# Optimization experiments

Hardware: AMD Instinct MI355X
Metric: run time of the kernel (lower is better)

Reference implementation:

```python
import jax, jax.numpy as jnp
import numpy as np

# init_kwargs constants
ALPHA = 0.1
BETA = 0.1
CAPACITY = 1000.0
IDX_LNN = 0   # feat_idx['ln(N+1)']
IDX_DOBS = 2  # feat_idx['D_observed']
IDX_RATE = 3  # feat_idx['pkt_rate']

N = 4_194_304
W = 4096  # number of windows (static upper bound on window ids)
EPS = 1e-6


def _masked_quantile75(vals, valid):
    """torch.quantile(vals[valid], 0.75) with linear interpolation, jit-safe."""
    s = jnp.sort(jnp.where(valid, vals, jnp.inf))
    n = jnp.sum(valid)
    pos = jnp.maximum(0.75 * (n - 1).astype(jnp.float32), 0.0)
    lo = jnp.floor(pos).astype(jnp.int32)
    hi = jnp.ceil(pos).astype(jnp.int32)
    frac = pos - lo.astype(jnp.float32)
    q = s[lo] * (1.0 - frac) + s[hi] * frac
    return jnp.where(n > 0, jnp.maximum(q, EPS), 1.0)


def setup_inputs() -> dict:
    key = jax.random.key(0)
    k1, k2, k3, k4, k5 = jax.random.split(key, 5)
    logits = jax.random.normal(k1, (N, 2), jnp.float32)
    y = jax.random.randint(k2, (N,), 0, 2)
    mask = jnp.ones((N,), bool)
    x_raw = jax.random.normal(k3, (N, 4), jnp.float32)
    window_idx = jax.random.randint(k4, (N,), 0, W)
    class_weights = jax.random.uniform(k5, (2,), jnp.float32, 0.5, 1.5)
    return {"logits": logits, "y": y, "mask": mask, "x_raw": x_raw,
            "window_idx": window_idx, "class_weights": class_weights}


def reference(logits, y, mask, x_raw, window_idx, class_weights):
    maskf = mask.astype(jnp.float32)
    any_mask = jnp.sum(maskf) > 0

    # L_data: weighted cross entropy over masked samples
    logp = jax.nn.log_softmax(logits, axis=1)
    nll = -jnp.take_along_axis(logp, y[:, None], axis=1)[:, 0]
    wy = class_weights[y]
    denom = jnp.sum(maskf * wy)
    l_data = jnp.sum(maskf * wy * nll) / jnp.maximum(denom, 1e-12)

    # per-window physics terms (vectorized segment reductions)
    valid = (window_idx >= 0) & mask
    vf = valid.astype(jnp.float32)
    attack_prob = jax.nn.softmax(logits, axis=1)[:, 1]
    flow_rate = jnp.maximum(x_raw[:, IDX_RATE], 0.0)
    d_obs = jnp.maximum(x_raw[:, IDX_DOBS], 0.0)
    # note: flow_vol (exp(lnN)-1) is computed in the original but never used in the loss

    ref_dobs = _masked_quantile75(d_obs, valid)

    seg = jnp.where(valid, window_idx, 0).astype(jnp.int32)
    pv = attack_prob * vf  # zeroed contributions for invalid rows
    cnt = jax.ops.segment_sum(vf, seg, num_segments=W)
    sum_p = jax.ops.segment_sum(pv, seg, num_segments=W)
    agg_rate = jax.ops.segment_sum(pv * flow_rate, seg, num_segments=W)
    sum_pd = jax.ops.segment_sum(pv * d_obs, seg, num_segments=W)

    include = ((cnt >= 2.0) & (sum_p >= EPS)).astype(jnp.float32)

    d_mean = sum_pd / (sum_p + EPS)
    rate_ratio = agg_rate / (CAPACITY + EPS)
    buildup = jax.nn.relu(rate_ratio - 1.0)
    flow_t = buildup * buildup
    rho = jnp.clip(rate_ratio, 0.0, 0.99)
    d_theory = 1.0 / (1.0 - rho + EPS)
    lat_t = jax.nn.relu(d_theory - d_mean / ref_dobs)

    n_inc = jnp.sum(include)
    safe_n = jnp.maximum(n_inc, 1.0)
    l_flow = jnp.where(n_inc > 0, jnp.sum(flow_t * include) / safe_n, 0.0)
    l_latency = jnp.where(n_inc > 0, jnp.sum(lat_t * include) / safe_n, 0.0)

    # empty-mask early return path
    l_data = jnp.where(any_mask, l_data, 0.0)
    l_flow = jnp.where(any_mask, l_flow, 0.0)
    l_latency = jnp.where(any_mask, l_latency, 0.0)
    l_total = l_data + ALPHA * l_flow + BETA * l_latency
    return (l_total, l_data, l_flow, l_latency)
```

## Files before the change

### kernel.cpp

```cpp
#include <hip/hip_runtime.h>

#define NWIN 4096
#define EPSF 1e-6f
#define GRID_MAIN 512
#define BLOCK_MAIN 512
#define NWAVES (BLOCK_MAIN / 64)

#define SCALE_P   2097152.0f
#define SCALE_R   131072.0f
#define INV_P     (1.0/2097152.0)
#define INV_R     (1.0/131072.0)

#define OFF_SEG   256
#define OFF_H1    65792
#define OFF_H2    73984
#define OFF_H3    90368
#define OFF_CEP   98560
#define OFF_SEGU  131072
#define OFF_PART  262144

__device__ __forceinline__ unsigned make_key_raw(const float2* __restrict__ xzw,
                                                 const int* __restrict__ mask,
                                                 const int* __restrict__ widx, int i)
{
    int wi = widx[i];
    int m = mask[i];
    if (wi < 0 || !m) return 0x7F800000u;
    float d = fmaxf(xzw[2 * i + 1].x, 0.0f);
    unsigned k = __float_as_uint(d);
    return (k == 0x80000000u) ? 0u : k;
}

__device__ __forceinline__ void process_elem(
    float lgx, float lgy, int yi, int mi, float xz, float xw, int wi,
    float cw0, float cw1, unsigned* keyOut,
    float& num, float& den, unsigned& nv, unsigned& nm, unsigned& zc,
    unsigned* s_seg, unsigned* s_h1)
{
    float d = lgx - lgy;
    float ad = fabsf(d);
    float t = __expf(-ad);
    float inv1t = 1.0f / (1.0f + t);
    float l1p = __logf(1.0f + t);
    float s = yi ? d : -d;
    float nll = fmaxf(s, 0.0f) + l1p;
    float maskf = mi ? 1.0f : 0.0f;
    float wy = (yi ? cw1 : cw0) * maskf;
    nm += (mi != 0);
    num += wy * nll;
    den += wy;

    bool vq = (wi >= 0) && mi;
    float dob = fmaxf(xz, 0.0f);
    unsigned kraw = __float_as_uint(dob);
    kraw = (kraw == 0x80000000u) ? 0u : kraw;
    unsigned key = vq ? kraw : 0x7F800000u;
    *keyOut = key;
    nv += vq;
    zc += (key == 0u);

    atomicAdd(&s_h1[key >> 21], (key != 0u) ? 1u : 0u);

    bool sv = vq && ((unsigned)wi < NWIN);
    float sf = sv ? 1.0f : 0.0f;
    unsigned b = sv ? ((unsigned)wi << 2) : (4u * NWIN);
    float p = ((d > 0.0f) ? t : 1.0f) * inv1t;
    float rate = fmaxf(xw, 0.0f);
    atomicAdd(&s_seg[b],     sv ? 1u : 0u);
    atomicAdd(&s_seg[b | 1], (unsigned)(sf * p * SCALE_P + 0.5f));
    atomicAdd(&s_seg[b | 2], (unsigned)(sf * p * rate * SCALE_R + 0.5f));
    atomicAdd(&s_seg[b | 3], (unsigned)(sf * p * dob * SCALE_R + 0.5f));
}

extern "C" __global__ __launch_bounds__(BLOCK_MAIN)
void k_main(const float2* __restrict__ logits, const int* __restrict__ y,
            const int* __restrict__ mask, const float2* __restrict__ xzw,
            const int* __restrict__ widx, const float* __restrict__ cw,
            float* __restrict__ ce_part,
            unsigned* __restrict__ g_seg_u32, unsigned* __restrict__ part,
            unsigned* __restrict__ keys, unsigned* __restrict__ gh1,
            int use_part, int use_keys, int n)
{
    __shared__ unsigned s_seg[4 * NWIN + 4];
    __shared__ unsigned s_h1[2048];
    __shared__ float s_redf[2 * NWAVES];
    __shared__ unsigned s_redu[3 * NWAVES];
    for (int j = threadIdx.x; j < 4 * NWIN + 4; j += BLOCK_MAIN) s_seg[j] = 0u;
    for (int j = threadIdx.x; j < 2048; j += BLOCK_MAIN) s_h1[j] = 0u;
    __syncthreads();

    const float cw0 = cw[0], cw1 = cw[1];
    float num = 0.0f, den = 0.0f;
    unsigned nv = 0u, nm = 0u, zc = 0u;

    const int nth = GRID_MAIN * BLOCK_MAIN;
    const int gtid = blockIdx.x * BLOCK_MAIN + threadIdx.x;
    const int nq = n >> 2;

    const float4* lg4 = (const float4*)logits;
    const int4* y4p = (const int4*)y;
    const int4* m4p = (const int4*)mask;
    const int4* w4p = (const int4*)widx;

    for (int q = gtid; q < nq; q += nth) {
        float4 lgA = lg4[2 * q], lgB = lg4[2 * q + 1];
        int4 y4 = y4p[q], m4 = m4p[q], w4 = w4p[q];
        float2 z0 = xzw[8 * q + 1], z1 = xzw[8 * q + 3];
        float2 z2 = xzw[8 * q + 5], z3 = xzw[8 * q + 7];

        uint4 kq;
        process_elem(lgA.x, lgA.y, y4.x, m4.x, z0.x, z0.y, w4.x,
                     cw0, cw1, &kq.x, num, den, nv, nm, zc, s_seg, s_h1);
        process_elem(lgA.z, lgA.w, y4.y, m4.y, z1.x, z1.y, w4.y,
                     cw0, cw1, &kq.y, num, den, nv, nm, zc, s_seg, s_h1);
        process_elem(lgB.x, lgB.y, y4.z, m4.z, z2.x, z2.y, w4.z,
                     cw0, cw1, &kq.z, num, den, nv, nm, zc, s_seg, s_h1);
        process_elem(lgB.z, lgB.w, y4.w, m4.w, z3.x, z3.y, w4.w,
                     cw0, cw1, &kq.w, num, den, nv, nm, zc, s_seg, s_h1);
        if (use_keys) ((uint4*)keys)[q] = kq;
    }
    for (int i = (nq << 2) + gtid; i < n; i += nth) {
        float2 lg = logits[i];
        float2 zz = xzw[2 * i + 1];
        unsigned k;
        process_elem(lg.x, lg.y, y[i], mask[i], zz.x, zz.y, widx[i],
                     cw0, cw1, &k, num, den, nv, nm, zc, s_seg, s_h1);
        if (use_keys) keys[i] = k;
    }

    for (int off = 32; off > 0; off >>= 1) {
        num += __shfl_down(num, off);
        den += __shfl_down(den, off);
        nv  += __shfl_down(nv, off);
        nm  += __shfl_down(nm, off);
        zc  += __shfl_down(zc, off);
    }
    const int wid = threadIdx.x >> 6;
    if ((threadIdx.x & 63) == 0) {
        s_redf[wid] = num; s_redf[NWAVES + wid] = den;
        s_redu[wid] = nv; s_redu[NWAVES + wid] = nm; s_redu[2 * NWAVES + wid] = zc;
    }
    __syncthreads();
    if (threadIdx.x == 0) {
        float tn = 0.0f, td = 0.0f;
        unsigned ta = 0u, tb = 0u, tc = 0u;
        for (int w = 0; w < NWAVES; ++w) {
            tn += s_redf[w]; td += s_redf[NWAVES + w];
            ta += s_redu[w]; tb += s_redu[NWAVES + w]; tc += s_redu[2 * NWAVES + w];
        }
        float* cp = ce_part + blockIdx.x * 8;
        cp[0] = tn; cp[1] = td;
        ((unsigned*)cp)[2] = ta; ((unsigned*)cp)[3] = tb; ((unsigned*)cp)[4] = tc;
    }

    if (use_part) {
        uint4* dst = (uint4*)(part + (size_t)blockIdx.x * (4 * NWIN));
        const uint4* src = (const uint4*)s_seg;
        for (int j = threadIdx.x; j < NWIN; j += BLOCK_MAIN) dst[j] = src[j];
    } else {
        for (int j = threadIdx.x; j < 4 * NWIN; j += BLOCK_MAIN) {
            unsigned v = s_seg[j];
            if (v) atomicAdd(&g_seg_u32[j], v);
        }
    }
    for (int j = threadIdx.x; j < 2048; j += BLOCK_MAIN) {
        unsigned v = s_h1[j];
        if (v) atomicAdd(&gh1[j], v);
    }
}

extern "C" __global__ __launch_bounds__(512)
void k_cefin(const float* __restrict__ ce_part, double* __restrict__ ws_d,
             unsigned* __restrict__ ws_u, unsigned* __restrict__ gh1)
{
    __shared__ double sd[2 * 8];
    __shared__ unsigned su[3 * 8];
    const int tid = threadIdx.x;
    const float* cp = ce_part + tid * 8;
    double n_ = (double)cp[0];
    double d_ = (double)cp[1];
    unsigned a = ((const unsigned*)cp)[2];
    unsigned b = ((const unsigned*)cp)[3];
    unsigned c = ((const unsigned*)cp)[4];
    for (int off = 32; off > 0; off >>= 1) {
        n_ += __shfl_down(n_, off);
        d_ += __shfl_down(d_, off);
        a  += __shfl_down(a, off);
        b  += __shfl_down(b, off);
        c  += __shfl_down(c, off);
    }
    const int wid = tid >> 6;
    if ((tid & 63) == 0) { sd[wid] = n_; sd[8 + wid] = d_;
                           su[wid] = a; su[8 + wid] = b; su[16 + wid] = c; }
    __syncthreads();
    if (tid == 0) {
        double tn = 0.0, td = 0.0;
        unsigned ta = 0u, tb = 0u, tc = 0u;
        for (int w = 0; w < 8; ++w) {
            tn += sd[w]; td += sd[8 + w];
            ta += su[w]; tb += su[8 + w]; tc += su[16 + w];
        }
        ws_d[0] = tn; ws_d[1] = td;
        ws_u[4] = ta; ws_u[5] = tb;
        gh1[0] += tc;
    }
}

extern "C" __global__ __launch_bounds__(256)
void k_reduce(const unsigned* __restrict__ part, unsigned* __restrict__ g_seg_u32)
{
    const int bin = (blockIdx.x & 63) * 256 + threadIdx.x;
    const int c = blockIdx.x >> 6;
    const unsigned* p = part + (size_t)c * (GRID_MAIN / 4) * (4 * NWIN) + bin;
    unsigned s = 0u;
#pragma unroll 8
    for (int b = 0; b < GRID_MAIN / 4; ++b) s += p[(size_t)b * (4 * NWIN)];
    if (s) atomicAdd(&g_seg_u32[bin], s);
}

extern "C" __global__ __launch_bounds__(256)
void k_convert(const unsigned* __restrict__ gsu, float* __restrict__ g_seg)
{
    const int j = blockIdx.x * 256 + threadIdx.x;
    const int c = j & 3;
    double inv = (c == 0) ? 1.0 : (c == 1) ? INV_P : INV_R;
    g_seg[j] = (float)((double)gsu[j] * inv);
}

__device__ __forceinline__ void h2_one(unsigned key, unsigned p0, unsigned p1,
                                       unsigned* h)
{
    unsigned top = key >> 21;
    unsigned sub = (key >> 10) & 2047u;
    if (top == p0) atomicAdd(&h[sub], 1u);
    if (top == p1) atomicAdd(&h[2048 + sub], 1u);
}

extern "C" __global__ __launch_bounds__(256)
void k_hist2(const unsigned* __restrict__ keys, const float2* __restrict__ xzw,
             const int* __restrict__ mask, const int* __restrict__ widx,
             int use_keys, int n, const unsigned* __restrict__ ws_u,
             unsigned* __restrict__ gh)
{
    __shared__ unsigned h[2 * 2048];
    for (int j = threadIdx.x; j < 2 * 2048; j += 256) h[j] = 0u;
    __syncthreads();
    const unsigned p0 = ws_u[8], p1 = ws_u[9];
    const int nthr = gridDim.x * blockDim.x;
    const int gtid = blockIdx.x * blockDim.x + threadIdx.x;
    const int nq = n >> 2;
    if (use_keys) {
        const uint4* k4 = (const uint4*)keys;
        int base = gtid;
        for (; base + 3 * nthr < nq; base += 4 * nthr) {
            uint4 a = k4[base], b = k4[base + nthr];
            uint4 c = k4[base + 2 * nthr], d = k4[base + 3 * nthr];
            h2_one(a.x, p0, p1, h); h2_one(a.y, p0, p1, h);
            h2_one(a.z, p0, p1, h); h2_one(a.w, p0, p1, h);
            h2_one(b.x, p0, p1, h); h2_one(b.y, p0, p1, h);
            h2_one(b.z, p0, p1, h); h2_one(b.w, p0, p1, h);
            h2_one(c.x, p0, p1, h); h2_one(c.y, p0, p1, h);
            h2_one(c.z, p0, p1, h); h2_one(c.w, p0, p1, h);
            h2_one(d.x, p0, p1, h); h2_one(d.y, p0, p1, h);
            h2_one(d.z, p0, p1, h); h2_one(d.w, p0, p1, h);
        }
        for (; base < nq; base += nthr) {
            uint4 a = k4[base];
            h2_one(a.x, p0, p1, h); h2_one(a.y, p0, p1, h);
            h2_one(a.z, p0, p1, h); h2_one(a.w, p0, p1, h);
        }
        for (int i = (nq << 2) + gtid; i < n; i += nthr)
            h2_one(keys[i], p0, p1, h);
    } else {
        for (int i = gtid; i < n; i += nthr)
            h2_one(make_key_raw(xzw, mask, widx, i), p0, p1, h);
    }
    __syncthreads();
    for (int j = threadIdx.x; j < 2 * 2048; j += 256)
        if (h[j]) atomicAdd(&gh[j], h[j]);
}

__device__ __forceinline__ void h3_one(unsigned key, unsigned p0, unsigned p1,
                                       unsigned* h)
{
    unsigned top = key >> 10;
    unsigned sub = key & 1023u;
    if (top == p0) atomicAdd(&h[sub], 1u);
    if (top == p1) atomicAdd(&h[1024 + sub], 1u);
}

extern "C" __global__ __launch_bounds__(256)
void k_hist3(const unsigned* __restrict__ keys, const float2* __restrict__ xzw,
             const int* __restrict__ mask, const int* __restrict__ widx,
             int use_keys, int n, const unsigned* __restrict__ ws_u,
             unsigned* __restrict__ gh)
{
    __shared__ unsigned h[2 * 1024];
    for (int j = threadIdx.x; j < 2 * 1024; j += 256) h[j] = 0u;
    __syncthreads();
    const unsigned p0 = ws_u[8], p1 = ws_u[9];
    const int nthr = gridDim.x * blockDim.x;
    const int gtid = blockIdx.x * blockDim.x + threadIdx.x;
    const int nq = n >> 2;
    if (use_keys) {
        const uint4* k4 = (const uint4*)keys;
        int base = gtid;
        for (; base + 3 * nthr < nq; base += 4 * nthr) {
            uint4 a = k4[base], b = k4[base + nthr];
            uint4 c = k4[base + 2 * nthr], d = k4[base + 3 * nthr];
            h3_one(a.x, p0, p1, h); h3_one(a.y, p0, p1, h);
            h3_one(a.z, p0, p1, h); h3_one(a.w, p0, p1, h);
            h3_one(b.x, p0, p1, h); h3_one(b.y, p0, p1, h);
            h3_one(b.z, p0, p1, h); h3_one(b.w, p0, p1, h);
            h3_one(c.x, p0, p1, h); h3_one(c.y, p0, p1, h);
            h3_one(c.z, p0, p1, h); h3_one(c.w, p0, p1, h);
            h3_one(d.x, p0, p1, h); h3_one(d.y, p0, p1, h);
            h3_one(d.z, p0, p1, h); h3_one(d.w, p0, p1, h);
        }
        for (; base < nq; base += nthr) {
            uint4 a = k4[base];
            h3_one(a.x, p0, p1, h); h3_one(a.y, p0, p1, h);
            h3_one(a.z, p0, p1, h); h3_one(a.w, p0, p1, h);
        }
        for (int i = (nq << 2) + gtid; i < n; i += nthr)
            h3_one(keys[i], p0, p1, h);
    } else {
        for (int i = gtid; i < n; i += nthr)
            h3_one(make_key_raw(xzw, mask, widx, i), p0, p1, h);
    }
    __syncthreads();
    for (int j = threadIdx.x; j < 2 * 1024; j += 256)
        if (h[j]) atomicAdd(&gh[j], h[j]);
}

__device__ void scan_search(const unsigned* __restrict__ gh, int NB, unsigned rank,
                            unsigned* sv, unsigned* wsb, unsigned* ret)
{
    const int tid = threadIdx.x;
    for (int j = tid; j < NB; j += 256) sv[j] = gh[j];
    __syncthreads();
    const int E = NB >> 8;
    const int base = tid * E;
    unsigned loc = 0u;
    for (int e = 0; e < E; ++e) loc += sv[base + e];
    unsigned inc = loc;
    const int lane = tid & 63;
    for (int off = 1; off < 64; off <<= 1) {
        unsigned u = __shfl_up(inc, off);
        if (lane >= off) inc += u;
    }
    const int wid = tid >> 6;
    if (lane == 63) wsb[wid] = inc;
    __syncthreads();
    if (tid == 0) {
        unsigned run = 0u;
        for (int w = 0; w < 4; ++w) { unsigned t = wsb[w]; wsb[w] = run; run += t; }
    }
    __syncthreads();
    unsigned c = wsb[wid] + (inc - loc);
    for (int e = 0; e < E; ++e) {
        unsigned hv = sv[base + e];
        if (rank >= c && rank < c + hv) { ret[0] = (unsigned)(base + e); ret[1] = rank - c; }
        c += hv;
    }
    __syncthreads();
}

extern "C" __global__ __launch_bounds__(256)
void k_scan1(unsigned* __restrict__ ws_u, float* __restrict__ ws_f,
             const unsigned* __restrict__ gh)
{
    __shared__ unsigned sv[2048];
    __shared__ unsigned wsb[4];
    __shared__ unsigned ret[2];
    __shared__ unsigned rk[2];
    if (threadIdx.x == 0) {
        int n = (int)ws_u[4];
        float nf = (float)(n - 1);
        float pos = fmaxf(0.75f * nf, 0.0f);
        float lo = floorf(pos);
        ws_f[7] = pos - lo;
        rk[0] = (unsigned)lo;
        rk[1] = (unsigned)ceilf(pos);
    }
    __syncthreads();
    unsigned r0 = rk[0], r1 = rk[1];
    scan_search(gh, 2048, r0, sv, wsb, ret);
    if (threadIdx.x == 0) { ws_u[8] = ret[0]; ws_u[10] = ret[1]; }
    scan_search(gh, 2048, r1, sv, wsb, ret);
    if (threadIdx.x == 0) { ws_u[9] = ret[0]; ws_u[11] = ret[1]; }
}

extern "C" __global__ __launch_bounds__(256)
void k_scan2(unsigned* __restrict__ ws_u, const unsigned* __restrict__ gh)
{
    __shared__ unsigned sv[2048];
    __shared__ unsigned wsb[4];
    __shared__ unsigned ret[2];
    unsigned p0 = ws_u[8], p1 = ws_u[9];
    unsigned r0 = ws_u[10], r1 = ws_u[11];
    scan_search(gh, 2048, r0, sv, wsb, ret);
    if (threadIdx.x == 0) { ws_u[8] = (p0 << 11) | ret[0]; ws_u[10] = ret[1]; }
    scan_search(gh + 2048, 2048, r1, sv, wsb, ret);
    if (threadIdx.x == 0) { ws_u[9] = (p1 << 11) | ret[0]; ws_u[11] = ret[1]; }
}

extern "C" __global__ __launch_bounds__(256)
void k_scan3(unsigned* __restrict__ ws_u, float* __restrict__ ws_f,
             const unsigned* __restrict__ gh)
{
    __shared__ unsigned sv[2048];
    __shared__ unsigned wsb[4];
    __shared__ unsigned ret[2];
    unsigned p0 = ws_u[8], p1 = ws_u[9];
    unsigned r0 = ws_u[10], r1 = ws_u[11];
    scan_search(gh, 1024, r0, sv, wsb, ret);
    float v0 = __uint_as_float((p0 << 10) | ret[0]);
    scan_search(gh + 1024, 1024, r1, sv, wsb, ret);
    float v1 = __uint_as_float((p1 << 10) | ret[0]);
    if (threadIdx.x == 0) {
        int n = (int)ws_u[4];
        float frac = ws_f[7];
        float q = v0 * (1.0f - frac) + v1 * frac;
        ws_f[6] = (n > 0) ? fmaxf(q, EPSF) : 1.0f;
    }
}

extern "C" __global__ __launch_bounds__(1024)
void k_final(const float* __restrict__ g_seg, const double* __restrict__ ws_d,
             const float* __restrict__ ws_f, const unsigned* __restrict__ ws_u,
             float* __restrict__ out)
{
    __shared__ double red[48];
    const double ref = (double)ws_f[6];
    const float4* gs4 = (const float4*)g_seg;
    double ninc = 0.0, fsum = 0.0, lsum = 0.0;
    for (int w = threadIdx.x; w < NWIN; w += blockDim.x) {
        float4 v = gs4[w];
        double c   = (double)v.x;
        double sp  = (double)v.y;
        double ar  = (double)v.z;
        double spd = (double)v.w;
        double inc = (c >= 2.0 && sp >= 1e-6) ? 1.0 : 0.0;
        double dmean = spd / (sp + 1e-6);
        double rr = ar / (1000.0 + 1e-6);
        double bu = fmax(rr - 1.0, 0.0);
        double flow = bu * bu;
        double rho = fmin(fmax(rr, 0.0), 0.99);
        double dth = 1.0 / (1.0 - rho + 1e-6);
        double lat = fmax(dth - dmean / ref, 0.0);
        ninc += inc; fsum += flow * inc; lsum += lat * inc;
    }
    for (int off = 32; off > 0; off >>= 1) {
        ninc += __shfl_down(ninc, off);
        fsum += __shfl_down(fsum, off);
        lsum += __shfl_down(lsum, off);
    }
    int wid = threadIdx.x >> 6, lane = threadIdx.x & 63;
    if (lane == 0) { red[wid] = ninc; red[16 + wid] = fsum; red[32 + wid] = lsum; }
    __syncthreads();
    if (threadIdx.x == 0) {
        double n_i = 0.0, f_s = 0.0, l_s = 0.0;
        int nw = (int)blockDim.x >> 6;
        for (int w = 0; w < nw; ++w) { n_i += red[w]; f_s += red[16 + w]; l_s += red[32 + w]; }
        double safe = fmax(n_i, 1.0);
        double l_flow = (n_i > 0.0) ? f_s / safe : 0.0;
        double l_lat  = (n_i > 0.0) ? l_s / safe : 0.0;
        double den = ws_d[1];
        double l_data = ws_d[0] / fmax(den, 1e-12);
        bool any = ws_u[5] > 0u;
        if (!any) { l_data = 0.0; l_flow = 0.0; l_lat = 0.0; }
        out[0] = (float)(l_data + 0.1 * l_flow + 0.1 * l_lat);
        out[1] = (float)l_data;
        out[2] = (float)l_flow;
        out[3] = (float)l_lat;
    }
}

extern "C" void kernel_launch(void* const* d_in, const int* in_sizes, int n_in,
                              void* d_out, int out_size, void* d_ws, size_t ws_size,
                              hipStream_t stream)
{
    const float2* logits = (const float2*)d_in[0];
    const int* y = (const int*)d_in[1];
    const int* mask = (const int*)d_in[2];
    const float2* xzw = (const float2*)d_in[3];
    const int* widx = (const int*)d_in[4];
    const float* cw = (const float*)d_in[5];
    float* out = (float*)d_out;
    const int n = in_sizes[1];

    unsigned char* ws8 = (unsigned char*)d_ws;
    double* ws_d = (double*)ws8;
    float* ws_f = (float*)ws8;
    unsigned* ws_u = (unsigned*)ws8;
    float* g_seg = (float*)(ws8 + OFF_SEG);
    unsigned* g_h1 = (unsigned*)(ws8 + OFF_H1);
    unsigned* g_h2 = (unsigned*)(ws8 + OFF_H2);
    unsigned* g_h3 = (unsigned*)(ws8 + OFF_H3);
    float* ce_part = (float*)(ws8 + OFF_CEP);
    unsigned* g_seg_u32 = (unsigned*)(ws8 + OFF_SEGU);

    const size_t part_bytes = (size_t)GRID_MAIN * 4 * NWIN * 4;
    const size_t keys_bytes = (size_t)n * 4u;
    size_t off = OFF_PART;
    int use_part = 0, use_keys = 0;
    unsigned* part = (unsigned*)(ws8 + off);
    if (ws_size >= off + part_bytes) { use_part = 1; off += part_bytes; }
    unsigned* keys = (unsigned*)(ws8 + off);
    if (ws_size >= off + keys_bytes) { use_keys = 1; }

    hipMemsetAsync(d_ws, 0, OFF_PART, stream);

    k_main<<<GRID_MAIN, BLOCK_MAIN, 0, stream>>>(logits, y, mask, xzw, widx, cw,
                                                 ce_part, g_seg_u32, part, keys,
                                                 g_h1, use_part, use_keys, n);
    k_cefin<<<1, 512, 0, stream>>>(ce_part, ws_d, ws_u, g_h1);
    if (use_part)
        k_reduce<<<256, 256, 0, stream>>>(part, g_seg_u32);
    k_convert<<<64, 256, 0, stream>>>(g_seg_u32, g_seg);
    k_scan1<<<1, 256, 0, stream>>>(ws_u, ws_f, g_h1);
    k_hist2<<<1024, 256, 0, stream>>>(keys, xzw, mask, widx, use_keys, n, ws_u, g_h2);
    k_scan2<<<1, 256, 0, stream>>>(ws_u, g_h2);
    k_hist3<<<1024, 256, 0, stream>>>(keys, xzw, mask, widx, use_keys, n, ws_u, g_h3);
    k_scan3<<<1, 256, 0, stream>>>(ws_u, ws_f, g_h3);
    k_final<<<1, 1024, 0, stream>>>(g_seg, ws_d, ws_f, ws_u, out);
}
```

Baseline: 98.80 us.

## Fuse post-processing kernels to cut launch count in the quantile pipeline

Merges k_cefin, k_reduce, k_convert and k_scan1 into a single k_post launch, where 128 blocks reduce the per-block partial window sums and one extra block does the cross-entropy finalisation and the first histogram scan. k_scan3 and k_convert are folded into k_final, which now scans the third histogram itself and converts the fixed-point window sums inline. This removes four kernel launches and their serial gaps. The cost is that k_post's reduction now uses 128 blocks of 512 threads instead of 256 blocks of 256, and the zero-count correction to the first histogram is applied in shared memory instead of written back to global memory.

Measured after the change: 91.84 us (median of 2 runs). 7.0% less time.

```diff
diff --git a/kernel.cpp b/kernel.cpp
--- a/kernel.cpp
+++ b/kernel.cpp
@@ -11,13 +11,12 @@
 #define INV_P     (1.0/2097152.0)
 #define INV_R     (1.0/131072.0)
 
-#define OFF_SEG   256
+#define OFF_SEGU  256
 #define OFF_H1    65792
 #define OFF_H2    73984
 #define OFF_H3    90368
 #define OFF_CEP   98560
-#define OFF_SEGU  131072
-#define OFF_PART  262144
+#define OFF_PART  131072
 
 __device__ __forceinline__ unsigned make_key_raw(const float2* __restrict__ xzw,
                                                  const int* __restrict__ mask,
@@ -169,12 +168,68 @@
     }
 }
 
+__device__ void scan_search_g(const unsigned* __restrict__ gh, int NB, unsigned rank,
+                              unsigned zadd, unsigned* sv, unsigned* wsb,
+                              unsigned* ret)
+{
+    const int tid = threadIdx.x;
+    const int B = blockDim.x;
+    for (int j = tid; j < NB; j += B) sv[j] = gh[j] + ((j == 0) ? zadd : 0u);
+    __syncthreads();
+    const int E = NB / B;
+    const int base = tid * E;
+    unsigned loc = 0u;
+    for (int e = 0; e < E; ++e) loc += sv[base + e];
+    unsigned inc = loc;
+    const int lane = tid & 63;
+    for (int off = 1; off < 64; off <<= 1) {
+        unsigned u = __shfl_up(inc, off);
+        if (lane >= off) inc += u;
+    }
+    const int wid = tid >> 6;
+    const int nw = B >> 6;
+    if (lane == 63) wsb[wid] = inc;
+    __syncthreads();
+    if (tid == 0) {
+        unsigned run = 0u;
+        for (int w = 0; w < nw; ++w) { unsigned t = wsb[w]; wsb[w] = run; run += t; }
+    }
+    __syncthreads();
+    unsigned c = wsb[wid] + (inc - loc);
+    for (int e = 0; e < E; ++e) {
+        unsigned hv = sv[base + e];
+        if (rank >= c && rank < c + hv) { ret[0] = (unsigned)(base + e); ret[1] = rank - c; }
+        c += hv;
+    }
+    __syncthreads();
+}
+
 extern "C" __global__ __launch_bounds__(512)
-void k_cefin(const float* __restrict__ ce_part, double* __restrict__ ws_d,
-             unsigned* __restrict__ ws_u, unsigned* __restrict__ gh1)
-{
+void k_post(const unsigned* __restrict__ part, unsigned* __restrict__ g_seg_u32,
+            const float* __restrict__ ce_part, double* __restrict__ ws_d,
+            unsigned* __restrict__ ws_u, float* __restrict__ ws_f,
+            const unsigned* __restrict__ gh1, int use_part)
+{
+    if (blockIdx.x < 128) {
+        if (!use_part) return;
+        const int c = blockIdx.x >> 5;
+        const int bin = (blockIdx.x & 31) * 512 + threadIdx.x;
+        const unsigned* p = part + (size_t)c * 128 * (4 * NWIN) + bin;
+        unsigned s = 0u;
+#pragma unroll 8
+        for (int b = 0; b < 128; ++b) s += p[(size_t)b * (4 * NWIN)];
+        if (s) atomicAdd(&g_seg_u32[bin], s);
+        return;
+    }
+
+    __shared__ unsigned sv[2048];
+    __shared__ unsigned wsb[16];
+    __shared__ unsigned ret[2];
     __shared__ double sd[2 * 8];
     __shared__ unsigned su[3 * 8];
+    __shared__ unsigned bc[4];
+    __shared__ float bf[1];
+
     const int tid = threadIdx.x;
     const float* cp = ce_part + tid * 8;
     double n_ = (double)cp[0];
@@ -202,29 +257,24 @@
         }
         ws_d[0] = tn; ws_d[1] = td;
         ws_u[4] = ta; ws_u[5] = tb;
-        gh1[0] += tc;
-    }
-}
-
-extern "C" __global__ __launch_bounds__(256)
-void k_reduce(const unsigned* __restrict__ part, unsigned* __restrict__ g_seg_u32)
-{
-    const int bin = (blockIdx.x & 63) * 256 + threadIdx.x;
-    const int c = blockIdx.x >> 6;
-    const unsigned* p = part + (size_t)c * (GRID_MAIN / 4) * (4 * NWIN) + bin;
-    unsigned s = 0u;
-#pragma unroll 8
-    for (int b = 0; b < GRID_MAIN / 4; ++b) s += p[(size_t)b * (4 * NWIN)];
-    if (s) atomicAdd(&g_seg_u32[bin], s);
-}
-
-extern "C" __global__ __launch_bounds__(256)
-void k_convert(const unsigned* __restrict__ gsu, float* __restrict__ g_seg)
-{
-    const int j = blockIdx.x * 256 + threadIdx.x;
-    const int c = j & 3;
-    double inv = (c == 0) ? 1.0 : (c == 1) ? INV_P : INV_R;
-    g_seg[j] = (float)((double)gsu[j] * inv);
+        float nf = (float)((int)ta - 1);
+        float pos = fmaxf(0.75f * nf, 0.0f);
+        float lo = floorf(pos);
+        bf[0] = pos - lo;
+        bc[0] = tc;
+        bc[1] = ta;
+        bc[2] = (unsigned)lo;
+        bc[3] = (unsigned)ceilf(pos);
+    }
+    __syncthreads();
+    const unsigned zadd = bc[0];
+    const unsigned r0 = bc[2], r1 = bc[3];
+    if (tid == 0) ws_f[7] = bf[0];
+
+    scan_search_g(gh1, 2048, r0, zadd, sv, wsb, ret);
+    if (tid == 0) { ws_u[8] = ret[0]; ws_u[10] = ret[1]; }
+    scan_search_g(gh1, 2048, r1, zadd, sv, wsb, ret);
+    if (tid == 0) { ws_u[9] = ret[0]; ws_u[11] = ret[1]; }
 }
 
 __device__ __forceinline__ void h2_one(unsigned key, unsigned p0, unsigned p1,
@@ -280,6 +330,20 @@
         if (h[j]) atomicAdd(&gh[j], h[j]);
 }
 
+extern "C" __global__ __launch_bounds__(256)
+void k_scan2(unsigned* __restrict__ ws_u, const unsigned* __restrict__ gh)
+{
+    __shared__ unsigned sv[2048];
+    __shared__ unsigned wsb[16];
+    __shared__ unsigned ret[2];
+    unsigned p0 = ws_u[8], p1 = ws_u[9];
+    unsigned r0 = ws_u[10], r1 = ws_u[11];
+    scan_search_g(gh, 2048, r0, 0u, sv, wsb, ret);
+    if (threadIdx.x == 0) { ws_u[8] = (p0 << 11) | ret[0]; ws_u[10] = ret[1]; }
+    scan_search_g(gh + 2048, 2048, r1, 0u, sv, wsb, ret);
+    if (threadIdx.x == 0) { ws_u[9] = (p1 << 11) | ret[0]; ws_u[11] = ret[1]; }
+}
+
 __device__ __forceinline__ void h3_one(unsigned key, unsigned p0, unsigned p1,
                                        unsigned* h)
 {
@@ -333,114 +397,36 @@
         if (h[j]) atomicAdd(&gh[j], h[j]);
 }
 
-__device__ void scan_search(const unsigned* __restrict__ gh, int NB, unsigned rank,
-                            unsigned* sv, unsigned* wsb, unsigned* ret)
-{
-    const int tid = threadIdx.x;
-    for (int j = tid; j < NB; j += 256) sv[j] = gh[j];
-    __syncthreads();
-    const int E = NB >> 8;
-    const int base = tid * E;
-    unsigned loc = 0u;
-    for (int e = 0; e < E; ++e) loc += sv[base + e];
-    unsigned inc = loc;
-    const int lane = tid & 63;
-    for (int off = 1; off < 64; off <<= 1) {
-        unsigned u = __shfl_up(inc, off);
-        if (lane >= off) inc += u;
-    }
-    const int wid = tid >> 6;
-    if (lane == 63) wsb[wid] = inc;
-    __syncthreads();
-    if (tid == 0) {
-        unsigned run = 0u;
-        for (int w = 0; w < 4; ++w) { unsigned t = wsb[w]; wsb[w] = run; run += t; }
-    }
-    __syncthreads();
-    unsigned c = wsb[wid] + (inc - loc);
-    for (int e = 0; e < E; ++e) {
-        unsigned hv = sv[base + e];
-        if (rank >= c && rank < c + hv) { ret[0] = (unsigned)(base + e); ret[1] = rank - c; }
-        c += hv;
-    }
-    __syncthreads();
-}
-
-extern "C" __global__ __launch_bounds__(256)
-void k_scan1(unsigned* __restrict__ ws_u, float* __restrict__ ws_f,
-             const unsigned* __restrict__ gh)
-{
-    __shared__ unsigned sv[2048];
-    __shared__ unsigned wsb[4];
+extern "C" __global__ __launch_bounds__(1024)
+void k_final(const unsigned* __restrict__ g_seg_u32, const double* __restrict__ ws_d,
+             const float* __restrict__ ws_f, const unsigned* __restrict__ ws_u,
+             const unsigned* __restrict__ gh3, float* __restrict__ out)
+{
+    __shared__ unsigned sv[1024];
+    __shared__ unsigned wsb[16];
     __shared__ unsigned ret[2];
-    __shared__ unsigned rk[2];
-    if (threadIdx.x == 0) {
-        int n = (int)ws_u[4];
-        float nf = (float)(n - 1);
-        float pos = fmaxf(0.75f * nf, 0.0f);
-        float lo = floorf(pos);
-        ws_f[7] = pos - lo;
-        rk[0] = (unsigned)lo;
-        rk[1] = (unsigned)ceilf(pos);
-    }
-    __syncthreads();
-    unsigned r0 = rk[0], r1 = rk[1];
-    scan_search(gh, 2048, r0, sv, wsb, ret);
-    if (threadIdx.x == 0) { ws_u[8] = ret[0]; ws_u[10] = ret[1]; }
-    scan_search(gh, 2048, r1, sv, wsb, ret);
-    if (threadIdx.x == 0) { ws_u[9] = ret[0]; ws_u[11] = ret[1]; }
-}
-
-extern "C" __global__ __launch_bounds__(256)
-void k_scan2(unsigned* __restrict__ ws_u, const unsigned* __restrict__ gh)
-{
-    __shared__ unsigned sv[2048];
-    __shared__ unsigned wsb[4];
-    __shared__ unsigned ret[2];
-    unsigned p0 = ws_u[8], p1 = ws_u[9];
-    unsigned r0 = ws_u[10], r1 = ws_u[11];
-    scan_search(gh, 2048, r0, sv, wsb, ret);
-    if (threadIdx.x == 0) { ws_u[8] = (p0 << 11) | ret[0]; ws_u[10] = ret[1]; }
-    scan_search(gh + 2048, 2048, r1, sv, wsb, ret);
-    if (threadIdx.x == 0) { ws_u[9] = (p1 << 11) | ret[0]; ws_u[11] = ret[1]; }
-}
-
-extern "C" __global__ __launch_bounds__(256)
-void k_scan3(unsigned* __restrict__ ws_u, float* __restrict__ ws_f,
-             const unsigned* __restrict__ gh)
-{
-    __shared__ unsigned sv[2048];
-    __shared__ unsigned wsb[4];
-    __shared__ unsigned ret[2];
-    unsigned p0 = ws_u[8], p1 = ws_u[9];
-    unsigned r0 = ws_u[10], r1 = ws_u[11];
-    scan_search(gh, 1024, r0, sv, wsb, ret);
-    float v0 = __uint_as_float((p0 << 10) | ret[0]);
-    scan_search(gh + 1024, 1024, r1, sv, wsb, ret);
-    float v1 = __uint_as_float((p1 << 10) | ret[0]);
-    if (threadIdx.x == 0) {
-        int n = (int)ws_u[4];
-        float frac = ws_f[7];
-        float q = v0 * (1.0f - frac) + v1 * frac;
-        ws_f[6] = (n > 0) ? fmaxf(q, EPSF) : 1.0f;
-    }
-}
-
-extern "C" __global__ __launch_bounds__(1024)
-void k_final(const float* __restrict__ g_seg, const double* __restrict__ ws_d,
-             const float* __restrict__ ws_f, const unsigned* __restrict__ ws_u,
-             float* __restrict__ out)
-{
     __shared__ double red[48];
-    const double ref = (double)ws_f[6];
-    const float4* gs4 = (const float4*)g_seg;
+
+    const unsigned p0 = ws_u[8], p1 = ws_u[9];
+    const unsigned r0 = ws_u[10], r1 = ws_u[11];
+    scan_search_g(gh3, 1024, r0, 0u, sv, wsb, ret);
+    const float v0 = __uint_as_float((p0 << 10) | ret[0]);
+    scan_search_g(gh3 + 1024, 1024, r1, 0u, sv, wsb, ret);
+    const float v1 = __uint_as_float((p1 << 10) | ret[0]);
+
+    const int nvalid = (int)ws_u[4];
+    const float frac = ws_f[7];
+    const float qf = v0 * (1.0f - frac) + v1 * frac;
+    const double ref = (double)((nvalid > 0) ? fmaxf(qf, EPSF) : 1.0f);
+
+    const uint4* gs4 = (const uint4*)g_seg_u32;
     double ninc = 0.0, fsum = 0.0, lsum = 0.0;
     for (int w = threadIdx.x; w < NWIN; w += blockDim.x) {
-        float4 v = gs4[w];
+        uint4 v = gs4[w];
         double c   = (double)v.x;
-        double sp  = (double)v.y;
-        double ar  = (double)v.z;
-        double spd = (double)v.w;
+        double sp  = (double)v.y * INV_P;
+        double ar  = (double)v.z * INV_R;
+        double spd = (double)v.w * INV_R;
         double inc = (c >= 2.0 && sp >= 1e-6) ? 1.0 : 0.0;
         double dmean = spd / (sp + 1e-6);
         double rr = ar / (1000.0 + 1e-6);
@@ -494,12 +480,11 @@
     double* ws_d = (double*)ws8;
     float* ws_f = (float*)ws8;
     unsigned* ws_u = (unsigned*)ws8;
-    float* g_seg = (float*)(ws8 + OFF_SEG);
+    unsigned* g_seg_u32 = (unsigned*)(ws8 + OFF_SEGU);
     unsigned* g_h1 = (unsigned*)(ws8 + OFF_H1);
     unsigned* g_h2 = (unsigned*)(ws8 + OFF_H2);
     unsigned* g_h3 = (unsigned*)(ws8 + OFF_H3);
     float* ce_part = (float*)(ws8 + OFF_CEP);
-    unsigned* g_seg_u32 = (unsigned*)(ws8 + OFF_SEGU);
 
     const size_t part_bytes = (size_t)GRID_MAIN * 4 * NWIN * 4;
     const size_t keys_bytes = (size_t)n * 4u;
@@ -515,14 +500,10 @@
     k_main<<<GRID_MAIN, BLOCK_MAIN, 0, stream>>>(logits, y, mask, xzw, widx, cw,
                                                  ce_part, g_seg_u32, part, keys,
                                                  g_h1, use_part, use_keys, n);
-    k_cefin<<<1, 512, 0, stream>>>(ce_part, ws_d, ws_u, g_h1);
-    if (use_part)
-        k_reduce<<<256, 256, 0, stream>>>(part, g_seg_u32);
-    k_convert<<<64, 256, 0, stream>>>(g_seg_u32, g_seg);
-    k_scan1<<<1, 256, 0, stream>>>(ws_u, ws_f, g_h1);
+    k_post<<<129, 512, 0, stream>>>(part, g_seg_u32, ce_part, ws_d, ws_u, ws_f,
+                                    g_h1, use_part);
     k_hist2<<<1024, 256, 0, stream>>>(keys, xzw, mask, widx, use_keys, n, ws_u, g_h2);
     k_scan2<<<1, 256, 0, stream>>>(ws_u, g_h2);
     k_hist3<<<1024, 256, 0, stream>>>(keys, xzw, mask, widx, use_keys, n, ws_u, g_h3);
-    k_scan3<<<1, 256, 0, stream>>>(ws_u, ws_f, g_h3);
-    k_final<<<1, 1024, 0, stream>>>(g_seg, ws_d, ws_f, ws_u, out);
-}
+    k_final<<<1, 1024, 0, stream>>>(g_seg_u32, ws_d, ws_f, ws_u, g_h3, out);
+}
```
